# Kernel optimization log

Measured on AMD Instinct MI355X. Metric: run time of the kernel, lower is better.

## Reference

```python
import jax, jax.numpy as jnp
import numpy as np
from jax import lax

B, C, H, W = 4, 512, 64, 64
C8 = C // 8
OUT = 256
BN_EPS = 1e-5


def setup_inputs() -> dict:
    key = jax.random.key(0)
    ks = jax.random.split(key, 12)
    s = lambda k, shape, fan: jax.random.normal(k, shape, jnp.float32) * (1.0 / np.sqrt(fan))
    return {
        "x": jax.random.normal(ks[0], (B, C, H, W), jnp.float32),
        "wq": s(ks[1], (C8, C), C), "bq": jnp.zeros((C8,), jnp.float32),
        "wk": s(ks[2], (C8, C), C), "bk": jnp.zeros((C8,), jnp.float32),
        "wv": s(ks[3], (C, C), C),  "bv": jnp.zeros((C,), jnp.float32),
        "ca_w1": s(ks[4], (C8, C), C),
        "ca_w2": s(ks[5], (C, C8), C8),
        "conv_w": s(ks[6], (OUT, C, 3, 3), C * 9),
        "bn_gamma": jnp.ones((OUT,), jnp.float32),
        "bn_beta": jnp.zeros((OUT,), jnp.float32),
        "bn_mean": jnp.zeros((OUT,), jnp.float32),
        "bn_var": jnp.ones((OUT,), jnp.float32),
    }


def reference(x, wq, bq, wk, bk, wv, bv, ca_w1, ca_w2, conv_w,
              bn_gamma, bn_beta, bn_mean, bn_var):
    b, c, h, w = x.shape
    n = h * w
    xf = x.reshape(b, c, n)  # [B,C,N]

    # ---- Position attention ----
    q = jnp.einsum('qc,bcn->bnq', wq, xf) + bq            # [B,N,C8]
    k = jnp.einsum('kc,bcn->bkn', wk, xf) + bk[:, None]   # [B,C8,N]
    energy = jnp.einsum('bnq,bqm->bnm', q, k)             # [B,N,N]
    attn = jax.nn.softmax(energy, axis=-1)
    v = jnp.einsum('vc,bcn->bvn', wv, xf) + bv[:, None]   # [B,C,N]
    # torch: bmm(value, attention^T) -> out[b,c,m] = sum_n v[b,c,n]*attn[b,m,n]
    pa = jnp.einsum('bcn,bmn->bcm', v, attn).reshape(b, c, h, w) + x

    # ---- Channel attention (SE-style, avg+max pooled, shared MLP) ----
    avg = jnp.mean(pa, axis=(2, 3))   # [B,C]
    mx = jnp.max(pa, axis=(2, 3))     # [B,C]
    fc = lambda z: jnp.einsum('oc,bc->bo', ca_w2,
                              jax.nn.relu(jnp.einsum('hc,bc->bh', ca_w1, z)))
    scale = jax.nn.sigmoid(fc(avg) + fc(mx))[:, :, None, None]
    ca = scale * pa

    # ---- Conv 3x3 + BN (eval mode) + ReLU ----
    y = lax.conv_general_dilated(ca, conv_w, (1, 1), 'SAME',
                                 dimension_numbers=('NCHW', 'OIHW', 'NCHW'))
    inv = lax.rsqrt(bn_var + BN_EPS)
    y = (y - bn_mean[:, None, None]) * (inv * bn_gamma)[:, None, None] + bn_beta[:, None, None]
    return jax.nn.relu(y)
```

## Files before the change

### kernel.cpp

```cpp
#include <hip/hip_runtime.h>

#define NB 4
#define CIN 512
#define NPIX 4096
#define CQK 64
#define COUT 256
#define PPIX 4356

typedef __bf16 bh16;
typedef _Float16 fh16;
typedef __attribute__((ext_vector_type(8))) __bf16 bf16x8;
typedef __attribute__((ext_vector_type(8))) _Float16 f16x8;
typedef __attribute__((ext_vector_type(16))) float f32x16;

#define AS1 __attribute__((address_space(1)))
#define AS3 __attribute__((address_space(3)))

__device__ __forceinline__ void glds16(const void* g, void* l) {
  __builtin_amdgcn_global_load_lds((const AS1 unsigned int*)g, (AS3 unsigned int*)l, 16, 0, 0);
}

__device__ __forceinline__ void lbar() {
  asm volatile("s_waitcnt lgkmcnt(0)\n\ts_barrier" ::: "memory");
}

__device__ __forceinline__ float fexp2(float x) {
#if __has_builtin(__builtin_amdgcn_exp2f)
  return __builtin_amdgcn_exp2f(x);
#else
  return __expf(x * 0.6931471805599453f);
#endif
}

__global__ __launch_bounds__(256) void transpose_bf_k(const float* __restrict__ src,
                                                      bh16* __restrict__ dst) {
  __shared__ float tile[64][65];
  const int b = blockIdx.z;
  const int n0 = blockIdx.x * 64;
  const int c0 = blockIdx.y * 64;
  const float* s = src + (size_t)b * CIN * NPIX;
  bh16* d = dst + (size_t)b * CIN * NPIX;
  const int t = threadIdx.x;
  const int q4 = (t & 15) * 4;
  const int rr = t >> 4;
#pragma unroll
  for (int i = 0; i < 4; i++) {
    const int c = rr + i * 16;
    const float4 v = *(const float4*)&s[(size_t)(c0 + c) * NPIX + n0 + q4];
    tile[q4 + 0][c] = v.x;
    tile[q4 + 1][c] = v.y;
    tile[q4 + 2][c] = v.z;
    tile[q4 + 3][c] = v.w;
  }
  __syncthreads();
#pragma unroll
  for (int i = 0; i < 4; i++) {
    const int n = rr + i * 16;
    union { bh16 h[4]; ushort4 u; } pk;
    pk.h[0] = (bh16)tile[n][q4 + 0];
    pk.h[1] = (bh16)tile[n][q4 + 1];
    pk.h[2] = (bh16)tile[n][q4 + 2];
    pk.h[3] = (bh16)tile[n][q4 + 3];
    *(ushort4*)(void*)&d[(size_t)(n0 + n) * CIN + c0 + q4] = pk.u;
  }
}

__global__ __launch_bounds__(256) void wcast_k(const float* __restrict__ wq,
                                               const float* __restrict__ wk,
                                               const float* __restrict__ wv,
                                               const float* __restrict__ bq,
                                               const float* __restrict__ bk,
                                               bh16* __restrict__ Wqk,
                                               bh16* __restrict__ wvb,
                                               float* __restrict__ bias128) {
  const int idx = blockIdx.x * 256 + threadIdx.x;
  if (idx < 65536) {
    Wqk[idx] = (bh16)(idx < 32768 ? wq[idx] : wk[idx - 32768]);
  } else {
    const int j = idx - 65536;
    wvb[j] = (bh16)wv[j];
  }
  if (idx < 128) bias128[idx] = idx < 64 ? bq[idx] : bk[idx - 64];
}

__global__ __launch_bounds__(256) void qk_proj_k(const bh16* __restrict__ xTb,
                                                 const bh16* __restrict__ Wqk,
                                                 const float* __restrict__ bias128,
                                                 bh16* __restrict__ Qb,
                                                 bh16* __restrict__ Kf) {
  const int blk = blockIdx.x;
  const int t = threadIdx.x;
  const int w = t >> 6, l31 = t & 31, hi = (t & 63) >> 5;
  __shared__ __align__(16) bh16 As[2][64 * 64];
  f32x16 acc[2];
#pragma unroll
  for (int nt = 0; nt < 2; nt++)
#pragma unroll
    for (int r = 0; r < 16; r++) acc[nt][r] = 0.0f;

#define QK_STAGE(kc, buf)                                                           \
  {                                                                                 \
    _Pragma("unroll") for (int i = 0; i < 2; i++) {                                 \
      const int s = i * 256 + t;                                                    \
      const int n = s >> 3, slot = s & 7;                                           \
      glds16(xTb + (size_t)(blk * 64 + n) * CIN + (kc) * 64 + (((slot + n) & 7) * 8), \
             &As[buf][(size_t)(i * 256 + w * 64) * 8]);                             \
    }                                                                               \
  }

  QK_STAGE(0, 0);
  __syncthreads();
  for (int kc = 0; kc < 8; kc++) {
    if (kc < 7) QK_STAGE(kc + 1, (kc + 1) & 1);
    const bh16* as = As[kc & 1];
#pragma unroll
    for (int ks = 0; ks < 4; ks++) {
      const bf16x8 bfr = *(const bf16x8*)(Wqk + (size_t)(w * 32 + l31) * CIN + kc * 64 + ks * 16 + hi * 8);
      const int kk = ks * 2 + hi;
#pragma unroll
      for (int nt = 0; nt < 2; nt++) {
        const int n = nt * 32 + l31;
        const bf16x8 a = *(const bf16x8*)&as[(size_t)(n * 8 + ((kk - n) & 7)) * 8];
        acc[nt] = __builtin_amdgcn_mfma_f32_32x32x16_bf16(a, bfr, acc[nt], 0, 0, 0);
      }
    }
    __syncthreads();
  }
#undef QK_STAGE
  const int o = w * 32 + l31;
  const float bo = bias128[o];
  if (w < 2) {
#pragma unroll
    for (int nt = 0; nt < 2; nt++)
#pragma unroll
      for (int r = 0; r < 16; r++) {
        const int nloc = nt * 32 + (r & 3) + 8 * (r >> 2) + 4 * hi;
        Qb[(size_t)(blk * 64 + nloc) * 64 + o] = (bh16)((acc[nt][r] + bo) * 1.44269504088896f);
      }
  } else {
    const int b = blk >> 6, jtile = blk & 63;
    const int k = o - 64, kg = k >> 3, k7 = k & 7;
    bh16* kdst = Kf + (((size_t)(b * 64 + jtile) * 8 + kg) * 64) * 8 + k7;
#pragma unroll
    for (int nt = 0; nt < 2; nt++)
#pragma unroll
      for (int r = 0; r < 16; r++) {
        const int j = nt * 32 + (r & 3) + 8 * (r >> 2) + 4 * hi;
        kdst[(size_t)j * 8] = (bh16)(acc[nt][r] + bo);
      }
  }
}

__global__ __launch_bounds__(256) void v_proj_k(const bh16* __restrict__ xTb,
                                                const bh16* __restrict__ wvb,
                                                const float* __restrict__ bv,
                                                bh16* __restrict__ Vf) {
  const int nblk = blockIdx.x;
  const int cblk = blockIdx.y;
  const int b = blockIdx.z;
  const int t = threadIdx.x;
  const int w = t >> 6, l31 = t & 31, hi = (t & 63) >> 5;
  __shared__ __align__(16) bh16 Bs[2][256 * 64];
  f32x16 acc[2][2];
#pragma unroll
  for (int mt = 0; mt < 2; mt++)
#pragma unroll
    for (int nt = 0; nt < 2; nt++)
#pragma unroll
      for (int r = 0; r < 16; r++) acc[mt][nt][r] = 0.0f;

#define V_STAGE(kc, buf)                                                              \
  {                                                                                   \
    _Pragma("unroll") for (int i = 0; i < 8; i++) {                                   \
      const int s = i * 256 + t;                                                      \
      const int n = s >> 3, slot = s & 7;                                             \
      glds16(xTb + (size_t)(b * NPIX + nblk * 256 + n) * CIN + (kc) * 64 + (((slot + n) & 7) * 8), \
             &Bs[buf][(size_t)(i * 256 + w * 64) * 8]);                               \
    }                                                                                 \
  }

  V_STAGE(0, 0);
  __syncthreads();
  for (int kc = 0; kc < 8; kc++) {
    if (kc < 7) V_STAGE(kc + 1, (kc + 1) & 1);
    const bh16* bs = Bs[kc & 1];
#pragma unroll
    for (int ks = 0; ks < 4; ks++) {
      const int kk = ks * 2 + hi;
      bf16x8 a[2], bfr[2];
#pragma unroll
      for (int mt = 0; mt < 2; mt++)
        a[mt] = *(const bf16x8*)(wvb + (size_t)(cblk * 64 + mt * 32 + l31) * CIN + kc * 64 + ks * 16 + hi * 8);
#pragma unroll
      for (int nt = 0; nt < 2; nt++) {
        const int n = w * 64 + nt * 32 + l31;
        bfr[nt] = *(const bf16x8*)&bs[(size_t)(n * 8 + ((kk - n) & 7)) * 8];
      }
#pragma unroll
      for (int mt = 0; mt < 2; mt++)
#pragma unroll
        for (int nt = 0; nt < 2; nt++)
          acc[mt][nt] = __builtin_amdgcn_mfma_f32_32x32x16_bf16(a[mt], bfr[nt], acc[mt][nt], 0, 0, 0);
    }
    __syncthreads();
  }
#undef V_STAGE
  const int ntile0 = nblk * 4 + w;
#pragma unroll
  for (int mt = 0; mt < 2; mt++)
#pragma unroll
    for (int r = 0; r < 16; r++) {
      const int c = cblk * 64 + mt * 32 + (r & 3) + 8 * (r >> 2) + 4 * hi;
      const float bvc = bv[c];
#pragma unroll
      for (int nt = 0; nt < 2; nt++) {
        const int nl = nt * 32 + l31;
        Vf[(((size_t)(b * 64 + ntile0) * 8 + (nl >> 3)) * 512 + c) * 8 + (nl & 7)] =
            (bh16)(acc[mt][nt][r] + bvc);
      }
    }
}

__global__ __launch_bounds__(256, 2) void attn1p_k(const bh16* __restrict__ Qb,
                                                   const bh16* __restrict__ Kf,
                                                   const bh16* __restrict__ Vf,
                                                   const float* __restrict__ x,
                                                   fh16* __restrict__ pa,
                                                   float* __restrict__ psum,
                                                   float* __restrict__ pmax) {
  const int id = blockIdx.x + 2 * (blockIdx.y + 64 * blockIdx.z);
  const int b = (id & 7) >> 1;
  const int cblk = id & 1;
  const int mblk = (id >> 3) * 64;
  const int t = threadIdx.x;
  const int w = t >> 6, l31 = t & 31, hi = (t >> 5) & 1;
  const int jhalf = w & 1, mhalf = w >> 1;
  __shared__ __align__(16) bh16 Ps[2][8 * 2 * 64 * 4];
  __shared__ float lred[4][32];
  __shared__ float linvL[64];

  bf16x8 qf[4];
  {
    const bh16* qrow = Qb + (size_t)(b * NPIX + mblk + mhalf * 32 + l31) * 64;
#pragma unroll
    for (int ks = 0; ks < 4; ks++) qf[ks] = *(const bf16x8*)(qrow + ks * 16 + hi * 8);
  }
  const bh16* kfb = Kf + (size_t)b * (64 * 8 * 64 * 8);
  const bh16* vfb = Vf + (size_t)b * (64 * 8 * 512 * 8);
  const int cbase = cblk * 256 + w * 64;

#define KADDR(tile, ks) (kfb + (((size_t)(tile) * 8 + (ks) * 2 + hi) * 64 + jhalf * 32 + l31) * 8)
#define VADDR(tile, ks, ct) (vfb + (((size_t)(tile) * 8 + (ks) * 2 + hi) * 512 + cbase + (ct) * 32 + l31) * 8)
#define PS_RD(f, base)                                                      \
  {                                                                         \
    f.u2[0] = *(const uint2*)&ps[(size_t)((base) + l31 * 4)];               \
    f.u2[1] = *(const uint2*)&ps[(size_t)((base) + 256 + l31 * 4)];         \
  }

  f32x16 acc[2][2];
#pragma unroll
  for (int mt = 0; mt < 2; mt++)
#pragma unroll
    for (int ct = 0; ct < 2; ct++)
#pragma unroll
      for (int r = 0; r < 16; r++) acc[mt][ct][r] = 0.0f;
  float4 lsacc;
  lsacc.x = 0.0f; lsacc.y = 0.0f; lsacc.z = 0.0f; lsacc.w = 0.0f;

  bf16x8 kf_nxt[4];
  bf16x8 vf_use[4][2];
  f32x16 s1;
  {
    bf16x8 k0[4];
#pragma unroll
    for (int ks = 0; ks < 4; ks++) {
      k0[ks] = *(const bf16x8*)KADDR(0, ks);
#pragma unroll
      for (int ct = 0; ct < 2; ct++) vf_use[ks][ct] = *(const bf16x8*)VADDR(0, ks, ct);
    }
#pragma unroll
    for (int ks = 0; ks < 4; ks++) kf_nxt[ks] = *(const bf16x8*)KADDR(1, ks);
#pragma unroll
    for (int r = 0; r < 16; r++) s1[r] = 0.0f;
#pragma unroll
    for (int ks = 0; ks < 4; ks++)
      s1 = __builtin_amdgcn_mfma_f32_32x32x16_bf16(k0[ks], qf[ks], s1, 0, 0, 0);
  }

  for (int it = 0; it < 64; it++) {
    f32x16 s1n;
#pragma unroll
    for (int r = 0; r < 16; r++) s1n[r] = 0.0f;
#pragma unroll
    for (int ks = 0; ks < 4; ks++)
      s1n = __builtin_amdgcn_mfma_f32_32x32x16_bf16(kf_nxt[ks], qf[ks], s1n, 0, 0, 0);
    {
      const int kt = (it + 2 < 64) ? it + 2 : 63;
#pragma unroll
      for (int ks = 0; ks < 4; ks++) kf_nxt[ks] = *(const bf16x8*)KADDR(kt, ks);
    }

    const bh16* ps = Ps[(it + 1) & 1];
    bh16* psw = Ps[it & 1];
    if (it) {
#pragma unroll
      for (int ks = 0; ks < 4; ks++) {
        const int ks2 = ks * 2 + hi;
        union { uint2 u2[2]; bf16x8 v; } f0, f1;
        PS_RD(f0, ks2 * 512);
        PS_RD(f1, ks2 * 512 + 128);
        acc[0][0] = __builtin_amdgcn_mfma_f32_32x32x16_bf16(f0.v, vf_use[ks][0], acc[0][0], 0, 0, 0);
        acc[0][1] = __builtin_amdgcn_mfma_f32_32x32x16_bf16(f0.v, vf_use[ks][1], acc[0][1], 0, 0, 0);
        {
          union { bh16 h[4]; uint2 u2; } pk;
#pragma unroll
          for (int q = 0; q < 4; q++) {
            const float p = fexp2(s1[ks * 4 + q]);
            lsacc[q] += p;
            pk.h[q] = (bh16)p;
          }
          *(uint2*)(void*)&psw[(size_t)((jhalf * 4 + ks) * 512 + hi * 256 + (mhalf * 32 + l31) * 4)] = pk.u2;
        }
        acc[1][0] = __builtin_amdgcn_mfma_f32_32x32x16_bf16(f1.v, vf_use[ks][0], acc[1][0], 0, 0, 0);
        acc[1][1] = __builtin_amdgcn_mfma_f32_32x32x16_bf16(f1.v, vf_use[ks][1], acc[1][1], 0, 0, 0);
        vf_use[ks][0] = *(const bf16x8*)VADDR(it, ks, 0);
        vf_use[ks][1] = *(const bf16x8*)VADDR(it, ks, 1);
      }
    } else {
#pragma unroll
      for (int g = 0; g < 4; g++) {
        union { bh16 h[4]; uint2 u2; } pk;
#pragma unroll
        for (int q = 0; q < 4; q++) {
          const float p = fexp2(s1[g * 4 + q]);
          lsacc[q] += p;
          pk.h[q] = (bh16)p;
        }
        *(uint2*)(void*)&psw[(size_t)((jhalf * 4 + g) * 512 + hi * 256 + (mhalf * 32 + l31) * 4)] = pk.u2;
      }
    }
    lbar();
    s1 = s1n;
  }
  {
    const bh16* ps = Ps[1];
#pragma unroll
    for (int ks = 0; ks < 4; ks++) {
      const int ks2 = ks * 2 + hi;
      union { uint2 u2[2]; bf16x8 v; } f0, f1;
      PS_RD(f0, ks2 * 512);
      PS_RD(f1, ks2 * 512 + 128);
      acc[0][0] = __builtin_amdgcn_mfma_f32_32x32x16_bf16(f0.v, vf_use[ks][0], acc[0][0], 0, 0, 0);
      acc[0][1] = __builtin_amdgcn_mfma_f32_32x32x16_bf16(f0.v, vf_use[ks][1], acc[0][1], 0, 0, 0);
      acc[1][0] = __builtin_amdgcn_mfma_f32_32x32x16_bf16(f1.v, vf_use[ks][0], acc[1][0], 0, 0, 0);
      acc[1][1] = __builtin_amdgcn_mfma_f32_32x32x16_bf16(f1.v, vf_use[ks][1], acc[1][1], 0, 0, 0);
    }
  }
#undef KADDR
#undef VADDR
#undef PS_RD

  float lsum = (lsacc.x + lsacc.y) + (lsacc.z + lsacc.w);
  lsum += __shfl_xor(lsum, 32);
  if (hi == 0) lred[w][l31] = lsum;
  __syncthreads();
  if (t < 64) linvL[t] = 1.0f / (lred[(t >> 5) * 2][t & 31] + lred[(t >> 5) * 2 + 1][t & 31]);
  __syncthreads();

  float csum[2] = {0.0f, 0.0f};
  float cmax[2] = {-1e30f, -1e30f};
#pragma unroll
  for (int mt = 0; mt < 2; mt++) {
#pragma unroll
    for (int g = 0; g < 4; g++) {
      const int mloc = mt * 32 + g * 8 + hi * 4;
      const float4 lv = *(const float4*)&linvL[mloc];
#pragma unroll
      for (int ct = 0; ct < 2; ct++) {
        const int c = cbase + ct * 32 + l31;
        const float4 xv = *(const float4*)&x[(size_t)(b * CIN + c) * NPIX + mblk + mloc];
        float r0 = acc[mt][ct][g * 4 + 0] * lv.x + xv.x;
        float r1 = acc[mt][ct][g * 4 + 1] * lv.y + xv.y;
        float r2 = acc[mt][ct][g * 4 + 2] * lv.z + xv.z;
        float r3 = acc[mt][ct][g * 4 + 3] * lv.w + xv.w;
        csum[ct] += (r0 + r1) + (r2 + r3);
        cmax[ct] = fmaxf(cmax[ct], fmaxf(fmaxf(r0, r1), fmaxf(r2, r3)));
        fh16* pd = pa + ((size_t)(b * NPIX) + mblk + mloc) * CIN + c;
        pd[0 * CIN] = (fh16)r0;
        pd[1 * CIN] = (fh16)r1;
        pd[2 * CIN] = (fh16)r2;
        pd[3 * CIN] = (fh16)r3;
      }
    }
  }
#pragma unroll
  for (int ct = 0; ct < 2; ct++) {
    csum[ct] += __shfl_xor(csum[ct], 32);
    cmax[ct] = fmaxf(cmax[ct], __shfl_xor(cmax[ct], 32));
  }
  if (hi == 0) {
    const int mb = mblk >> 6;
#pragma unroll
    for (int ct = 0; ct < 2; ct++) {
      const int c = cbase + ct * 32 + l31;
      psum[((size_t)b * 64 + mb) * CIN + c] = csum[ct];
      pmax[((size_t)b * 64 + mb) * CIN + c] = cmax[ct];
    }
  }
}

__global__ __launch_bounds__(256) void mlp2_k(const float* __restrict__ psum,
                                              const float* __restrict__ pmax,
                                              const float* __restrict__ w1,
                                              const float* __restrict__ w2,
                                              float* __restrict__ scale) {
  const int b = blockIdx.x;
  const int t = threadIdx.x;
  __shared__ float avg_l[CIN], max_l[CIN], hbuf[128];
#pragma unroll
  for (int h = 0; h < 2; h++) {
    const int c = t + h * 256;
    float s = 0.0f, m = -1e30f;
#pragma unroll
    for (int k = 0; k < 64; k++) {
      s += psum[((size_t)b * 64 + k) * CIN + c];
      m = fmaxf(m, pmax[((size_t)b * 64 + k) * CIN + c]);
    }
    avg_l[c] = s * (1.0f / 4096.0f);
    max_l[c] = m;
  }
  __syncthreads();
  if (t < 128) {
    const float* src = (t < 64) ? avg_l : max_l;
    const int o = t & 63;
    float sacc = 0.0f;
    for (int c = 0; c < CIN; c += 4) {
      const float4 wv = *(const float4*)&w1[o * CIN + c];
      sacc += wv.x * src[c] + wv.y * src[c + 1] + wv.z * src[c + 2] + wv.w * src[c + 3];
    }
    hbuf[t] = fmaxf(sacc, 0.0f);
  }
  __syncthreads();
#pragma unroll
  for (int h = 0; h < 2; h++) {
    const int c = t + h * 256;
    float sacc = 0.0f;
#pragma unroll
    for (int k = 0; k < 64; k += 4) {
      const float4 wv = *(const float4*)&w2[c * 64 + k];
      sacc += wv.x * (hbuf[k] + hbuf[64 + k]) + wv.y * (hbuf[k + 1] + hbuf[64 + k + 1]) +
              wv.z * (hbuf[k + 2] + hbuf[64 + k + 2]) + wv.w * (hbuf[k + 3] + hbuf[64 + k + 3]);
    }
    scale[b * CIN + c] = 1.0f / (1.0f + __expf(-sacc));
  }
}

__global__ __launch_bounds__(256) void pack_k(const fh16* __restrict__ pa,
                                              const float* __restrict__ scl,
                                              fh16* __restrict__ pab) {
  const int b = blockIdx.y;
  const int n0 = blockIdx.x * 8;
  const int t = threadIdx.x;
  __shared__ float sc[CIN];
#pragma unroll
  for (int h = 0; h < 2; h++) sc[t + h * 256] = scl[b * CIN + t + h * 256];
  __syncthreads();
  const int c2 = t * 2;
  const float s0 = sc[c2], s1 = sc[c2 + 1];
#pragma unroll
  for (int j = 0; j < 8; j++) {
    const int n = n0 + j;
    const int pp = ((n >> 6) + 1) * 66 + (n & 63) + 1;
    union { fh16 h[2]; unsigned int u; } v, o;
    v.u = *(const unsigned int*)(pa + ((size_t)b * NPIX + n) * CIN + c2);
    o.h[0] = (fh16)((float)v.h[0] * s0);
    o.h[1] = (fh16)((float)v.h[1] * s1);
    *(unsigned int*)(void*)(pab + ((size_t)b * PPIX + pp) * CIN + c2) = o.u;
  }
}

__global__ __launch_bounds__(256) void bzero_k(fh16* __restrict__ pab) {
  const int t = threadIdx.x;
  const int p = blockIdx.x * 4 + (t >> 6);
  const int b = blockIdx.y;
  int pp;
  if (p < 66) pp = p;
  else if (p < 132) pp = 65 * 66 + (p - 66);
  else if (p < 196) pp = (p - 131) * 66;
  else pp = (p - 195) * 66 + 65;
  uint4 z = {0u, 0u, 0u, 0u};
  *(uint4*)(void*)(pab + ((size_t)b * PPIX + pp) * CIN + (t & 63) * 8) = z;
}

__global__ __launch_bounds__(256) void wpack_k(const float* __restrict__ cw,
                                               fh16* __restrict__ wp) {
  const int slot = blockIdx.x * 256 + threadIdx.x;
  const int oblk = slot / 36864;
  const int r1 = slot - oblk * 36864;
  const int chunk = r1 / 1152;
  const int r2 = r1 - chunk * 1152;
  const int tap = r2 >> 7;
  const int r3 = r2 & 127;
  const int h = r3 >> 6;
  const int o = r3 & 63;
  const size_t sbase = (size_t)(oblk * 64 + o) * 4608 + (size_t)(chunk * 16 + h * 8) * 9 + tap;
  union { fh16 h8[8]; uint4 u4; } pk;
#pragma unroll
  for (int i = 0; i < 8; i++) pk.h8[i] = (fh16)cw[sbase + (size_t)i * 9];
  *(uint4*)(void*)(wp + (size_t)slot * 8) = pk.u4;
}

__global__ __launch_bounds__(256) void conv_mfma_k(const fh16* __restrict__ pab,
                                                   const fh16* __restrict__ wp,
                                                   const float* __restrict__ gamma,
                                                   const float* __restrict__ beta,
                                                   const float* __restrict__ mean,
                                                   const float* __restrict__ var,
                                                   float* __restrict__ out) {
  const int y0 = blockIdx.x * 4;
  const int oblk = blockIdx.y;
  const int b = blockIdx.z;
  const int t = threadIdx.x;
  const int w = t >> 6, lane = t & 63, l31 = lane & 31, hi = lane >> 5;
  __shared__ __align__(16) fh16 Xs[2][416 * 16];
  __shared__ __align__(16) fh16 Ws[2][9 * 64 * 16];
  __shared__ float sb[64], bb[64];
  if (t < 64) {
    const int o = oblk * 64 + t;
    const float inv = rsqrtf(var[o] + 1e-5f);
    const float sc = inv * gamma[o];
    sb[t] = sc;
    bb[t] = beta[o] - mean[o] * sc;
  }
  f32x16 o00, o01, o10, o11;
#pragma unroll
  for (int r = 0; r < 16; r++) { o00[r] = 0.0f; o01[r] = 0.0f; o10[r] = 0.0f; o11[r] = 0.0f; }

  const fh16* xbase = pab + ((size_t)b * PPIX + y0 * 66) * CIN + (size_t)(lane & 31) * CIN + (lane >> 5) * 8;
  const fh16* wbase = wp + (size_t)oblk * 32 * 9216 + lane * 8;

#define STAGE(chunk, buf)                                                        \
  {                                                                              \
    const fh16* xs = xbase + (chunk) * 16;                                       \
    for (int i = w; i < 13; i += 4)                                              \
      glds16(xs + (size_t)i * 32 * CIN, &Xs[buf][i * 512]);                      \
    const fh16* wsrc = wbase + (size_t)(chunk) * 9216;                           \
    for (int i = w; i < 18; i += 4)                                              \
      glds16(wsrc + (size_t)i * 512, &Ws[buf][i * 512]);                         \
  }

  STAGE(0, 0);
  __syncthreads();
  for (int chunk = 0; chunk < 32; chunk++) {
    if (chunk < 31) STAGE(chunk + 1, (chunk + 1) & 1);
    const fh16* xs = Xs[chunk & 1];
    const fh16* ws = Ws[chunk & 1];
#pragma unroll
    for (int tap = 0; tap < 9; tap++) {
      const int ky = tap / 3, kx = tap - ky * 3;
      const f16x8 a0 = *(const f16x8*)&ws[tap * 1024 + hi * 512 + l31 * 8];
      const f16x8 a1 = *(const f16x8*)&ws[tap * 1024 + hi * 512 + (32 + l31) * 8];
      const int row0 = (w + ky) * 66 + l31 + kx;
      const int row1 = row0 + 32;
      const f16x8 b0 = *(const f16x8*)&xs[(row0 >> 5) * 512 + hi * 256 + (row0 & 31) * 8];
      const f16x8 b1 = *(const f16x8*)&xs[(row1 >> 5) * 512 + hi * 256 + (row1 & 31) * 8];
      o00 = __builtin_amdgcn_mfma_f32_32x32x16_f16(a0, b0, o00, 0, 0, 0);
      o01 = __builtin_amdgcn_mfma_f32_32x32x16_f16(a0, b1, o01, 0, 0, 0);
      o10 = __builtin_amdgcn_mfma_f32_32x32x16_f16(a1, b0, o10, 0, 0, 0);
      o11 = __builtin_amdgcn_mfma_f32_32x32x16_f16(a1, b1, o11, 0, 0, 0);
    }
    __syncthreads();
  }
#undef STAGE

  const f32x16* accs[2][2] = {{&o00, &o01}, {&o10, &o11}};
#pragma unroll
  for (int mt = 0; mt < 2; mt++) {
#pragma unroll
    for (int nt = 0; nt < 2; nt++) {
      const f32x16& A = *accs[mt][nt];
#pragma unroll
      for (int r = 0; r < 16; r++) {
        const int cl = mt * 32 + (r & 3) + 8 * (r >> 2) + 4 * hi;
        const int pix = nt * 32 + l31;
        const float y = A[r] * sb[cl] + bb[cl];
        out[((size_t)(b * COUT + oblk * 64 + cl)) * NPIX + (y0 + w) * 64 + pix] = fmaxf(y, 0.0f);
      }
    }
  }
}

extern "C" void kernel_launch(void* const* d_in, const int* in_sizes, int n_in,
                              void* d_out, int out_size, void* d_ws, size_t ws_size,
                              hipStream_t stream) {
  (void)in_sizes; (void)n_in; (void)out_size; (void)ws_size;
  const float* x        = (const float*)d_in[0];
  const float* wq       = (const float*)d_in[1];
  const float* bq       = (const float*)d_in[2];
  const float* wk       = (const float*)d_in[3];
  const float* bk       = (const float*)d_in[4];
  const float* wv       = (const float*)d_in[5];
  const float* bv       = (const float*)d_in[6];
  const float* ca_w1    = (const float*)d_in[7];
  const float* ca_w2    = (const float*)d_in[8];
  const float* conv_w   = (const float*)d_in[9];
  const float* bn_gamma = (const float*)d_in[10];
  const float* bn_beta  = (const float*)d_in[11];
  const float* bn_mean  = (const float*)d_in[12];
  const float* bn_var   = (const float*)d_in[13];
  float* out = (float*)d_out;

  float* ws = (float*)d_ws;
  fh16*  pa      = (fh16*)ws;
  float* psum    = ws + 4194304;
  float* pmax    = ws + 4325376;
  bh16*  Vf      = (bh16*)(ws + 8388608);
  fh16*  wpck    = (fh16*)(ws + 8388608);
  bh16*  Qb      = (bh16*)(ws + 12582912);
  bh16*  Kf      = (bh16*)(ws + 13107200);
  bh16*  xTb     = (bh16*)(ws + 13631488);
  fh16*  pab     = (fh16*)(ws + 13631488);
  bh16*  Wqk     = (bh16*)(ws + 17825792);
  bh16*  wvb     = (bh16*)(ws + 17858560);
  float* bias128 = ws + 17989632;
  float* scl     = ws + 18104320;

  wcast_k<<<dim3(1280, 1, 1), 256, 0, stream>>>(wq, wk, wv, bq, bk, Wqk, wvb, bias128);
  transpose_bf_k<<<dim3(NPIX / 64, CIN / 64, NB), 256, 0, stream>>>(x, xTb);
  qk_proj_k<<<dim3(256, 1, 1), 256, 0, stream>>>(xTb, Wqk, bias128, Qb, Kf);
  v_proj_k<<<dim3(16, 8, NB), 256, 0, stream>>>(xTb, wvb, bv, Vf);
  attn1p_k<<<dim3(2, 64, NB), 256, 0, stream>>>(Qb, Kf, Vf, x, pa, psum, pmax);
  bzero_k<<<dim3(65, NB, 1), 256, 0, stream>>>(pab);
  mlp2_k<<<dim3(NB, 1, 1), 256, 0, stream>>>(psum, pmax, ca_w1, ca_w2, scl);
  pack_k<<<dim3(NPIX / 8, NB, 1), 256, 0, stream>>>(pa, scl, pab);
  wpack_k<<<dim3(576, 1, 1), 256, 0, stream>>>(conv_w, wpck);
  conv_mfma_k<<<dim3(16, 4, NB), 256, 0, stream>>>(pab, wpck, bn_gamma, bn_beta,
                                                   bn_mean, bn_var, out);
}
```

Before: 322.6 us.

## Repartition PV warp tiling to 32 rows x 128 channels per warp

Each warp in the attention PV stage now owns a 32-row by 128-channel output tile (four channel tiles sharing one P fragment) instead of 64 rows by 64 channels. The P buffer in LDS is relaid out so each lane reads its fragment with a single 16-byte load rather than two 8-byte reads. This halves P reads from LDS per MFMA but doubles V register fragments and global V loads per warp. It also adds a cross-warp LDS reduction for the channel pooling partials, which needs an extra barrier.

```diff
diff --git a/kernel.cpp b/kernel.cpp
--- a/kernel.cpp
+++ b/kernel.cpp
@@ -235,9 +235,11 @@
   const int t = threadIdx.x;
   const int w = t >> 6, l31 = t & 31, hi = (t >> 5) & 1;
   const int jhalf = w & 1, mhalf = w >> 1;
-  __shared__ __align__(16) bh16 Ps[2][8 * 2 * 64 * 4];
+  const int mh2 = w & 1, cq = w >> 1;
+  __shared__ __align__(16) bh16 Ps[2][8 * 64 * 8];
   __shared__ float lred[4][32];
   __shared__ float linvL[64];
+  __shared__ float cpool_s[4][4][32], cpool_m[4][4][32];
 
   bf16x8 qf[4];
   {
@@ -247,28 +249,21 @@
   }
   const bh16* kfb = Kf + (size_t)b * (64 * 8 * 64 * 8);
   const bh16* vfb = Vf + (size_t)b * (64 * 8 * 512 * 8);
-  const int cbase = cblk * 256 + w * 64;
+  const int cbase = cblk * 256 + cq * 128;
 
 #define KADDR(tile, ks) (kfb + (((size_t)(tile) * 8 + (ks) * 2 + hi) * 64 + jhalf * 32 + l31) * 8)
 #define VADDR(tile, ks, ct) (vfb + (((size_t)(tile) * 8 + (ks) * 2 + hi) * 512 + cbase + (ct) * 32 + l31) * 8)
-#define PS_RD(f, base)                                                      \
-  {                                                                         \
-    f.u2[0] = *(const uint2*)&ps[(size_t)((base) + l31 * 4)];               \
-    f.u2[1] = *(const uint2*)&ps[(size_t)((base) + 256 + l31 * 4)];         \
-  }
-
-  f32x16 acc[2][2];
-#pragma unroll
-  for (int mt = 0; mt < 2; mt++)
-#pragma unroll
-    for (int ct = 0; ct < 2; ct++)
-#pragma unroll
-      for (int r = 0; r < 16; r++) acc[mt][ct][r] = 0.0f;
+
+  f32x16 acc[4];
+#pragma unroll
+  for (int ct = 0; ct < 4; ct++)
+#pragma unroll
+    for (int r = 0; r < 16; r++) acc[ct][r] = 0.0f;
   float4 lsacc;
   lsacc.x = 0.0f; lsacc.y = 0.0f; lsacc.z = 0.0f; lsacc.w = 0.0f;
 
   bf16x8 kf_nxt[4];
-  bf16x8 vf_use[4][2];
+  bf16x8 vf_use[4][4];
   f32x16 s1;
   {
     bf16x8 k0[4];
@@ -276,7 +271,7 @@
     for (int ks = 0; ks < 4; ks++) {
       k0[ks] = *(const bf16x8*)KADDR(0, ks);
 #pragma unroll
-      for (int ct = 0; ct < 2; ct++) vf_use[ks][ct] = *(const bf16x8*)VADDR(0, ks, ct);
+      for (int ct = 0; ct < 4; ct++) vf_use[ks][ct] = *(const bf16x8*)VADDR(0, ks, ct);
     }
 #pragma unroll
     for (int ks = 0; ks < 4; ks++) kf_nxt[ks] = *(const bf16x8*)KADDR(1, ks);
@@ -306,11 +301,9 @@
 #pragma unroll
       for (int ks = 0; ks < 4; ks++) {
         const int ks2 = ks * 2 + hi;
-        union { uint2 u2[2]; bf16x8 v; } f0, f1;
-        PS_RD(f0, ks2 * 512);
-        PS_RD(f1, ks2 * 512 + 128);
-        acc[0][0] = __builtin_amdgcn_mfma_f32_32x32x16_bf16(f0.v, vf_use[ks][0], acc[0][0], 0, 0, 0);
-        acc[0][1] = __builtin_amdgcn_mfma_f32_32x32x16_bf16(f0.v, vf_use[ks][1], acc[0][1], 0, 0, 0);
+        const bf16x8 pf = *(const bf16x8*)&ps[(size_t)(ks2 * 64 + mh2 * 32 + l31) * 8];
+        acc[0] = __builtin_amdgcn_mfma_f32_32x32x16_bf16(pf, vf_use[ks][0], acc[0], 0, 0, 0);
+        acc[1] = __builtin_amdgcn_mfma_f32_32x32x16_bf16(pf, vf_use[ks][1], acc[1], 0, 0, 0);
         {
           union { bh16 h[4]; uint2 u2; } pk;
 #pragma unroll
@@ -319,12 +312,12 @@
             lsacc[q] += p;
             pk.h[q] = (bh16)p;
           }
-          *(uint2*)(void*)&psw[(size_t)((jhalf * 4 + ks) * 512 + hi * 256 + (mhalf * 32 + l31) * 4)] = pk.u2;
+          *(uint2*)(void*)&psw[(size_t)((jhalf * 4 + ks) * 64 + mhalf * 32 + l31) * 8 + hi * 4] = pk.u2;
         }
-        acc[1][0] = __builtin_amdgcn_mfma_f32_32x32x16_bf16(f1.v, vf_use[ks][0], acc[1][0], 0, 0, 0);
-        acc[1][1] = __builtin_amdgcn_mfma_f32_32x32x16_bf16(f1.v, vf_use[ks][1], acc[1][1], 0, 0, 0);
-        vf_use[ks][0] = *(const bf16x8*)VADDR(it, ks, 0);
-        vf_use[ks][1] = *(const bf16x8*)VADDR(it, ks, 1);
+        acc[2] = __builtin_amdgcn_mfma_f32_32x32x16_bf16(pf, vf_use[ks][2], acc[2], 0, 0, 0);
+        acc[3] = __builtin_amdgcn_mfma_f32_32x32x16_bf16(pf, vf_use[ks][3], acc[3], 0, 0, 0);
+#pragma unroll
+        for (int ct = 0; ct < 4; ct++) vf_use[ks][ct] = *(const bf16x8*)VADDR(it, ks, ct);
       }
     } else {
 #pragma unroll
@@ -336,7 +329,7 @@
           lsacc[q] += p;
           pk.h[q] = (bh16)p;
         }
-        *(uint2*)(void*)&psw[(size_t)((jhalf * 4 + g) * 512 + hi * 256 + (mhalf * 32 + l31) * 4)] = pk.u2;
+        *(uint2*)(void*)&psw[(size_t)((jhalf * 4 + g) * 64 + mhalf * 32 + l31) * 8 + hi * 4] = pk.u2;
       }
     }
     lbar();
@@ -347,18 +340,14 @@
 #pragma unroll
     for (int ks = 0; ks < 4; ks++) {
       const int ks2 = ks * 2 + hi;
-      union { uint2 u2[2]; bf16x8 v; } f0, f1;
-      PS_RD(f0, ks2 * 512);
-      PS_RD(f1, ks2 * 512 + 128);
-      acc[0][0] = __builtin_amdgcn_mfma_f32_32x32x16_bf16(f0.v, vf_use[ks][0], acc[0][0], 0, 0, 0);
-      acc[0][1] = __builtin_amdgcn_mfma_f32_32x32x16_bf16(f0.v, vf_use[ks][1], acc[0][1], 0, 0, 0);
-      acc[1][0] = __builtin_amdgcn_mfma_f32_32x32x16_bf16(f1.v, vf_use[ks][0], acc[1][0], 0, 0, 0);
-      acc[1][1] = __builtin_amdgcn_mfma_f32_32x32x16_bf16(f1.v, vf_use[ks][1], acc[1][1], 0, 0, 0);
+      const bf16x8 pf = *(const bf16x8*)&ps[(size_t)(ks2 * 64 + mh2 * 32 + l31) * 8];
+#pragma unroll
+      for (int ct = 0; ct < 4; ct++)
+        acc[ct] = __builtin_amdgcn_mfma_f32_32x32x16_bf16(pf, vf_use[ks][ct], acc[ct], 0, 0, 0);
     }
   }
 #undef KADDR
 #undef VADDR
-#undef PS_RD
 
   float lsum = (lsacc.x + lsacc.y) + (lsacc.z + lsacc.w);
   lsum += __shfl_xor(lsum, 32);
@@ -367,44 +356,49 @@
   if (t < 64) linvL[t] = 1.0f / (lred[(t >> 5) * 2][t & 31] + lred[(t >> 5) * 2 + 1][t & 31]);
   __syncthreads();
 
-  float csum[2] = {0.0f, 0.0f};
-  float cmax[2] = {-1e30f, -1e30f};
-#pragma unroll
-  for (int mt = 0; mt < 2; mt++) {
-#pragma unroll
-    for (int g = 0; g < 4; g++) {
-      const int mloc = mt * 32 + g * 8 + hi * 4;
-      const float4 lv = *(const float4*)&linvL[mloc];
-#pragma unroll
-      for (int ct = 0; ct < 2; ct++) {
-        const int c = cbase + ct * 32 + l31;
-        const float4 xv = *(const float4*)&x[(size_t)(b * CIN + c) * NPIX + mblk + mloc];
-        float r0 = acc[mt][ct][g * 4 + 0] * lv.x + xv.x;
-        float r1 = acc[mt][ct][g * 4 + 1] * lv.y + xv.y;
-        float r2 = acc[mt][ct][g * 4 + 2] * lv.z + xv.z;
-        float r3 = acc[mt][ct][g * 4 + 3] * lv.w + xv.w;
-        csum[ct] += (r0 + r1) + (r2 + r3);
-        cmax[ct] = fmaxf(cmax[ct], fmaxf(fmaxf(r0, r1), fmaxf(r2, r3)));
-        fh16* pd = pa + ((size_t)(b * NPIX) + mblk + mloc) * CIN + c;
-        pd[0 * CIN] = (fh16)r0;
-        pd[1 * CIN] = (fh16)r1;
-        pd[2 * CIN] = (fh16)r2;
-        pd[3 * CIN] = (fh16)r3;
-      }
-    }
-  }
-#pragma unroll
-  for (int ct = 0; ct < 2; ct++) {
+  float csum[4] = {0.0f, 0.0f, 0.0f, 0.0f};
+  float cmax[4] = {-1e30f, -1e30f, -1e30f, -1e30f};
+#pragma unroll
+  for (int g = 0; g < 4; g++) {
+    const int mloc = mh2 * 32 + g * 8 + hi * 4;
+    const float4 lv = *(const float4*)&linvL[mloc];
+#pragma unroll
+    for (int ct = 0; ct < 4; ct++) {
+      const int c = cbase + ct * 32 + l31;
+      const float4 xv = *(const float4*)&x[(size_t)(b * CIN + c) * NPIX + mblk + mloc];
+      float r0 = acc[ct][g * 4 + 0] * lv.x + xv.x;
+      float r1 = acc[ct][g * 4 + 1] * lv.y + xv.y;
+      float r2 = acc[ct][g * 4 + 2] * lv.z + xv.z;
+      float r3 = acc[ct][g * 4 + 3] * lv.w + xv.w;
+      csum[ct] += (r0 + r1) + (r2 + r3);
+      cmax[ct] = fmaxf(cmax[ct], fmaxf(fmaxf(r0, r1), fmaxf(r2, r3)));
+      fh16* pd = pa + ((size_t)(b * NPIX) + mblk + mloc) * CIN + c;
+      pd[0 * CIN] = (fh16)r0;
+      pd[1 * CIN] = (fh16)r1;
+      pd[2 * CIN] = (fh16)r2;
+      pd[3 * CIN] = (fh16)r3;
+    }
+  }
+#pragma unroll
+  for (int ct = 0; ct < 4; ct++) {
     csum[ct] += __shfl_xor(csum[ct], 32);
     cmax[ct] = fmaxf(cmax[ct], __shfl_xor(cmax[ct], 32));
   }
   if (hi == 0) {
+#pragma unroll
+    for (int ct = 0; ct < 4; ct++) {
+      cpool_s[w][ct][l31] = csum[ct];
+      cpool_m[w][ct][l31] = cmax[ct];
+    }
+  }
+  __syncthreads();
+  if ((w & 1) == 0 && hi == 0) {
     const int mb = mblk >> 6;
 #pragma unroll
-    for (int ct = 0; ct < 2; ct++) {
+    for (int ct = 0; ct < 4; ct++) {
       const int c = cbase + ct * 32 + l31;
-      psum[((size_t)b * 64 + mb) * CIN + c] = csum[ct];
-      pmax[((size_t)b * 64 + mb) * CIN + c] = cmax[ct];
+      psum[((size_t)b * 64 + mb) * CIN + c] = cpool_s[w][ct][l31] + cpool_s[w + 1][ct][l31];
+      pmax[((size_t)b * 64 + mb) * CIN + c] = fmaxf(cpool_m[w][ct][l31], cpool_m[w + 1][ct][l31]);
     }
   }
 }
```

Result: slower. 356.3 us (+10.4%).
